# Optimization experiments

Hardware: AMD Instinct MI355X
Metric: run time of the kernel (lower is better)

## Reference

```python
import jax, jax.numpy as jnp
import numpy as np
from jax.scipy.special import logsumexp

N, S, D, C = 64, 512, 768, 32


def setup_inputs() -> dict:
    key = jax.random.key(0)
    k1, k2, k3, k4, k5 = jax.random.split(key, 5)
    X = jax.random.normal(k1, (N, S, D), dtype=jnp.float32)
    W = jax.random.normal(k2, (D, C), dtype=jnp.float32) * 0.02
    T = jax.random.normal(k3, (C, C), dtype=jnp.float32) * 0.1
    # one-hot labels [N,S,C]
    lab_idx = jax.random.randint(k4, (N, S), 0, C)
    labels = jax.nn.one_hot(lab_idx, C, dtype=jnp.float32)
    # pad_mask: 1 for first `length` positions, 0 after (lengths in [S//2, S])
    lengths = jax.random.randint(k5, (N,), S // 2, S + 1)
    pad_mask = (jnp.arange(S)[None, :] < lengths[:, None]).astype(jnp.float32)
    return {"X": X, "W": W, "T": T, "labels": labels, "pad_mask": pad_mask}


def _crf_nll(X, W, T, labels, pad_mask):
    npots = jnp.einsum("nsd,dc->nsc", X, W)  # [N,S,C]
    m = pad_mask[..., None]                   # [N,S,1]

    # Faithful replication of the in-place masking loop:
    # prev starts as the ORIGINAL last timestep (t-1 == -1 at t=0 in torch).
    def prop(prev, xs):
        nt, mt = xs
        new = (1.0 - mt) * prev + mt * nt
        return new, new

    _, np_t = jax.lax.scan(
        prop, npots[:, -1, :],
        (jnp.swapaxes(npots, 0, 1), jnp.swapaxes(m, 0, 1)))
    npots = jnp.swapaxes(np_t, 0, 1)  # [N,S,C]

    # Backward messages: msgs[i,j] = lse_k(np[i+1,k] + T[j,k] + msgs[i+1,k]) * mask[i+1]
    def bwd(msg_next, xs):
        np_next, m_next = xs  # [N,C], [N,1]
        new = logsumexp(np_next[:, None, :] + T[None, :, :] + msg_next[:, None, :],
                        axis=-1) * m_next
        return new, new

    xs = (jnp.swapaxes(npots[:, 1:, :], 0, 1), jnp.swapaxes(m[:, 1:, :], 0, 1))
    init = jnp.zeros((npots.shape[0], npots.shape[2]), dtype=npots.dtype)
    _, msgs = jax.lax.scan(bwd, init, xs, reverse=True)
    bwd0 = msgs[0]  # message at position 0

    logZ = logsumexp(npots[:, 0, :] + bwd0, axis=-1)  # [N]

    # Unnormalized gold-path score
    score = jnp.sum(jnp.sum(npots * labels, axis=-1) * pad_mask, axis=-1)
    labels_idx = jnp.argmax(labels, axis=-1)          # [N,S]
    trans = T[labels_idx[:, :-1]]                     # [N,S-1,C]
    score = score + jnp.sum(
        jnp.sum(trans * labels[:, 1:, :], axis=-1) * pad_mask[:, 1:], axis=-1)

    return -jnp.mean(score - logZ)


def reference(X, W, T, labels, pad_mask):
    return _crf_nll(X, W, T, labels, pad_mask)
```

## Files before the change

### kernel.cpp

```cpp
#include <hip/hip_runtime.h>
#include <hip/hip_bf16.h>
#include <math.h>

#define N_ 64
#define S_ 512
#define D_ 768
#define C_ 32
#define KCH 16
#define LC 32
#define WT_LD 776
#define BKC 96
#define ROWS_PB 128

typedef __attribute__((ext_vector_type(8))) short bf16x8;
typedef __attribute__((ext_vector_type(4))) float f32x4;
typedef __attribute__((ext_vector_type(16))) float f32x16;

__device__ inline ushort f2bf(float x) {
    unsigned int b = __builtin_bit_cast(unsigned int, x);
    return (ushort)((b + 0x7FFFu + ((b >> 16) & 1u)) >> 16);
}

__device__ inline unsigned cvt_pk_bf16(float lo, float hi) {
    unsigned r;
    asm("v_cvt_pk_bf16_f32 %0, %1, %2" : "=v"(r) : "v"(lo), "v"(hi));
    return r;
}

__device__ __forceinline__ void gload_lds16(const float* g, float* l) {
    __builtin_amdgcn_global_load_lds(
        (const __attribute__((address_space(1))) unsigned int*)g,
        (__attribute__((address_space(3))) unsigned int*)l, 16, 0, 0);
}

__global__ __launch_bounds__(512) void gemm_npots_mfma(const float* __restrict__ X,
                                                       const float* __restrict__ W,
                                                       float* __restrict__ npots) {
    __shared__ float  Xs[2][ROWS_PB * BKC];
    __shared__ ushort WtS[C_ * WT_LD];
    const int tid = threadIdx.x;
    const int w   = tid >> 6;
    const int l   = tid & 63;
    const int lr  = l & 15;
    const int q   = l >> 4;
    const int row0 = blockIdx.x * ROWS_PB;

    for (int i = tid; i < D_ * C_; i += 512) {
        const int k = i >> 5, c = i & 31;
        WtS[c * WT_LD + k] = f2bf(W[i]);
    }

    #define STAGE(ck, buf)                                                        \
        {                                                                         \
            _Pragma("unroll")                                                     \
            for (int i_ = 0; i_ < 6; ++i_) {                                      \
                const int G   = (w * 6 + i_) * 64 + l;                            \
                const int row = G / 24;                                           \
                const int g   = G - row * 24;                                     \
                const int gs  = g ^ (row & 7);                                    \
                gload_lds16(X + (size_t)(row0 + row) * D_ + (ck) * BKC + gs * 4,  \
                            &Xs[buf][G * 4]);                                     \
            }                                                                     \
        }

    STAGE(0, 0);
    asm volatile("s_waitcnt vmcnt(0)" ::: "memory");
    __syncthreads();

    f32x4 acc0 = {0.f, 0.f, 0.f, 0.f};
    f32x4 acc1 = {0.f, 0.f, 0.f, 0.f};
    const int myrow = w * 16 + lr;
    const int sw    = myrow & 7;
    const ushort* wb0 = &WtS[lr * WT_LD];
    const ushort* wb1 = &WtS[(lr + 16) * WT_LD];

    for (int c = 0; c < D_ / BKC; ++c) {
        if (c < D_ / BKC - 1) STAGE(c + 1, (c + 1) & 1);
        const float* xb = Xs[c & 1];
        #pragma unroll
        for (int kk = 0; kk < 3; ++kk) {
            const int g0 = 8 * kk + 2 * q;
            const f32x4 alo = *(const f32x4*)&xb[(myrow * 24 + (g0 ^ sw)) * 4];
            const f32x4 ahi = *(const f32x4*)&xb[(myrow * 24 + ((g0 + 1) ^ sw)) * 4];
            union { unsigned u[4]; bf16x8 v; } af;
            af.u[0] = cvt_pk_bf16(alo[0], alo[1]);
            af.u[1] = cvt_pk_bf16(alo[2], alo[3]);
            af.u[2] = cvt_pk_bf16(ahi[0], ahi[1]);
            af.u[3] = cvt_pk_bf16(ahi[2], ahi[3]);
            const int kg = c * BKC + kk * 32 + q * 8;
            const bf16x8 b0 = *(const bf16x8*)(wb0 + kg);
            const bf16x8 b1 = *(const bf16x8*)(wb1 + kg);
            acc0 = __builtin_amdgcn_mfma_f32_16x16x32_bf16(af.v, b0, acc0, 0, 0, 0);
            acc1 = __builtin_amdgcn_mfma_f32_16x16x32_bf16(af.v, b1, acc1, 0, 0, 0);
        }
        asm volatile("s_waitcnt vmcnt(0)" ::: "memory");
        __syncthreads();
    }
    #undef STAGE

    const int r0 = row0 + w * 16 + q * 4;
    #pragma unroll
    for (int reg = 0; reg < 4; ++reg) {
        npots[(size_t)(r0 + reg) * C_ + lr]      = acc0[reg];
        npots[(size_t)(r0 + reg) * C_ + lr + 16] = acc1[reg];
    }
}

__global__ __launch_bounds__(128) void chunk_score(const float* __restrict__ npots,
                                                   const float* __restrict__ pad,
                                                   const float* __restrict__ T,
                                                   const float* __restrict__ labels,
                                                   float* __restrict__ Bg,
                                                   float* __restrict__ chunk_ls,
                                                   float* __restrict__ scores_p) {
    const int n = blockIdx.x, k = blockIdx.y;
    const int tid = threadIdx.x;
    const int l = tid & 63;
    __shared__ __align__(16) float e_lds[LC * C_];

    if (tid >= 64) {
        const int tb = k * LC;
        int best = 0;
        if (l <= LC) {
            const int t = tb - 1 + l;
            if (t >= 0) {
                const float* lrow = labels + ((size_t)n * S_ + t) * C_;
                float bv = lrow[0];
                #pragma unroll
                for (int c = 1; c < C_; ++c) {
                    const float x = lrow[c];
                    if (x > bv) { bv = x; best = c; }
                }
            }
        }
        const int cur = __shfl(best, l + 1);
        float v = 0.f;
        if (l < LC) {
            const int t = tb + l;
            const float p = pad[(size_t)n * S_ + t];
            v = p * npots[((size_t)n * S_ + t) * C_ + cur];
            if (t >= 1) v = fmaf(p, T[best * C_ + cur], v);
        }
        #pragma unroll
        for (int o = 32; o >= 1; o >>= 1) v += __shfl_xor(v, o);
        if (l == 0) scores_p[n * KCH + k] = v;
        return;
    }

    const int cc = l & 31;
    const int h  = l >> 5;

    const float* pm = pad + (size_t)n * S_;
    float ls = 0.f;
    for (int t = l; t < S_; t += 64) ls += pm[t];
    #pragma unroll
    for (int o = 32; o >= 1; o >>= 1) ls += __shfl_xor(ls, o);
    const int len = (int)(ls + 0.5f);

    float* Bout = Bg + ((size_t)n * KCH + k) * (C_ * C_);
    const int lo = k * LC;
    const int hi = min(lo + LC, len - 1);

    if (lo >= len - 1) {
        #pragma unroll
        for (int qq = 0; qq < 16; ++qq) {
            const int row = (qq & 3) + 8 * (qq >> 2) + 4 * h;
            Bout[row * C_ + cc] = (row == cc) ? 1.f : 0.f;
        }
        if (l == 0) chunk_ls[n * KCH + k] = 0.f;
        return;
    }

    const int cnt = hi - lo;

    const float* npn = npots + ((size_t)n * S_ + lo) * C_;
    for (int qd = l * 4; qd < cnt * C_; qd += 256) {
        const float4 v = *(const float4*)(npn + qd);
        *(float4*)&e_lds[qd] = make_float4(expf(v.x), expf(v.y), expf(v.z), expf(v.w));
    }
    asm volatile("s_waitcnt lgkmcnt(0)" ::: "memory");

    float glo[8], ghi[8];
    {
        const float* el = e_lds + (size_t)(cnt - 1) * C_;
        #pragma unroll
        for (int j = 0; j < 8; ++j) {
            const int kk = 8 * h + j;
            glo[j] = el[kk]      * expf(T[kk * C_ + cc]);
            ghi[j] = el[kk + 16] * expf(T[(kk + 16) * C_ + cc]);
        }
    }

    if (cnt == 1) {
        #pragma unroll
        for (int j = 0; j < 8; ++j) {
            Bout[(8 * h + j) * C_ + cc]      = glo[j];
            Bout[(8 * h + j + 16) * C_ + cc] = ghi[j];
        }
        if (l == 0) chunk_ls[n * KCH + k] = 0.f;
        return;
    }

    union { unsigned u[4]; bf16x8 v; } ETalo, ETahi, blo, bhi;
    #pragma unroll
    for (int t = 0; t < 4; ++t) {
        const int kk = 8 * h + 2 * t;
        ETalo.u[t] = cvt_pk_bf16(expf(T[cc * C_ + kk]),      expf(T[cc * C_ + kk + 1]));
        ETahi.u[t] = cvt_pk_bf16(expf(T[cc * C_ + kk + 16]), expf(T[cc * C_ + kk + 17]));
        blo.u[t]   = cvt_pk_bf16(glo[2 * t], glo[2 * t + 1]);
        bhi.u[t]   = cvt_pk_bf16(ghi[2 * t], ghi[2 * t + 1]);
    }

    float logscale = 0.f;
    int it = 0;
    for (int i = hi - 2; i >= lo; --i) {
        f32x16 d = {};
        d = __builtin_amdgcn_mfma_f32_32x32x16_bf16(ETalo.v, blo.v, d, 0, 0, 0);
        d = __builtin_amdgcn_mfma_f32_32x32x16_bf16(ETahi.v, bhi.v, d, 0, 0, 0);

        const float* ep = e_lds + (i - lo) * C_ + 4 * h;
        const float4 e0 = *(const float4*)(ep);
        const float4 e1 = *(const float4*)(ep + 8);
        const float4 e2 = *(const float4*)(ep + 16);
        const float4 e3 = *(const float4*)(ep + 24);
        float sd[16];
        sd[0]  = d[0]  * e0.x;  sd[1]  = d[1]  * e0.y;  sd[2]  = d[2]  * e0.z;  sd[3]  = d[3]  * e0.w;
        sd[4]  = d[4]  * e1.x;  sd[5]  = d[5]  * e1.y;  sd[6]  = d[6]  * e1.z;  sd[7]  = d[7]  * e1.w;
        sd[8]  = d[8]  * e2.x;  sd[9]  = d[9]  * e2.y;  sd[10] = d[10] * e2.z;  sd[11] = d[11] * e2.w;
        sd[12] = d[12] * e3.x;  sd[13] = d[13] * e3.y;  sd[14] = d[14] * e3.z;  sd[15] = d[15] * e3.w;

        if ((++it & 7) == 0) {
            float m = sd[0];
            #pragma unroll
            for (int qq = 1; qq < 16; ++qq) m = fmaxf(m, sd[qq]);
            #pragma unroll
            for (int o = 32; o >= 1; o >>= 1) m = fmaxf(m, __shfl_xor(m, o));
            logscale += logf(m);
            const float inv = 1.f / m;
            #pragma unroll
            for (int qq = 0; qq < 16; ++qq) sd[qq] *= inv;
        }

        if (i > lo) {
            const unsigned w0 = cvt_pk_bf16(sd[0],  sd[1]);
            const unsigned w1 = cvt_pk_bf16(sd[2],  sd[3]);
            const unsigned w2 = cvt_pk_bf16(sd[4],  sd[5]);
            const unsigned w3 = cvt_pk_bf16(sd[6],  sd[7]);
            const unsigned w4 = cvt_pk_bf16(sd[8],  sd[9]);
            const unsigned w5 = cvt_pk_bf16(sd[10], sd[11]);
            const unsigned w6 = cvt_pk_bf16(sd[12], sd[13]);
            const unsigned w7 = cvt_pk_bf16(sd[14], sd[15]);
            const unsigned x0 = (unsigned)__shfl_xor((int)w0, 32);
            const unsigned x1 = (unsigned)__shfl_xor((int)w1, 32);
            const unsigned x2 = (unsigned)__shfl_xor((int)w2, 32);
            const unsigned x3 = (unsigned)__shfl_xor((int)w3, 32);
            const unsigned x4 = (unsigned)__shfl_xor((int)w4, 32);
            const unsigned x5 = (unsigned)__shfl_xor((int)w5, 32);
            const unsigned x6 = (unsigned)__shfl_xor((int)w6, 32);
            const unsigned x7 = (unsigned)__shfl_xor((int)w7, 32);
            blo.u[0] = h ? x2 : w0;
            blo.u[1] = h ? x3 : w1;
            blo.u[2] = h ? w2 : x0;
            blo.u[3] = h ? w3 : x1;
            bhi.u[0] = h ? x6 : w4;
            bhi.u[1] = h ? x7 : w5;
            bhi.u[2] = h ? w6 : x4;
            bhi.u[3] = h ? w7 : x5;
        } else {
            #pragma unroll
            for (int qq = 0; qq < 16; ++qq)
                Bout[((qq & 3) + 8 * (qq >> 2) + 4 * h) * C_ + cc] = sd[qq];
        }
    }
    if (l == 0) chunk_ls[n * KCH + k] = logscale;
}

__global__ __launch_bounds__(64) void combine_logZ(const float* __restrict__ npots,
                                                   const float* __restrict__ pad,
                                                   const float* __restrict__ Bg,
                                                   const float* __restrict__ chunk_ls,
                                                   float* __restrict__ logZ) {
    const int n = blockIdx.x;
    const int l = threadIdx.x;
    const int r = l & 31;
    const int h = l >> 5;
    __shared__ __align__(16) float w_lds[32];

    const float* pm = pad + (size_t)n * S_;
    float ls = 0.f;
    for (int t = l; t < S_; t += 64) ls += pm[t];
    #pragma unroll
    for (int o = 32; o >= 1; o >>= 1) ls += __shfl_xor(ls, o);
    const int len = (int)(ls + 0.5f);

    float cls = (l < KCH) ? chunk_ls[n * KCH + l] : 0.f;
    #pragma unroll
    for (int o = 32; o >= 1; o >>= 1) cls += __shfl_xor(cls, o);

    const float np_last = npots[((size_t)n * S_ + (len - 1)) * C_ + r];
    float m0 = np_last;
    #pragma unroll
    for (int o = 32; o >= 1; o >>= 1) m0 = fmaxf(m0, __shfl_xor(m0, o));
    float logscale = m0 + cls;
    if (h == 0) w_lds[r] = expf(np_last - m0);
    __syncthreads();

    float bv[16];
    {
        const float* Brow = Bg + ((size_t)n * KCH + (KCH - 1)) * (C_ * C_) + r * C_ + h * 16;
        #pragma unroll
        for (int t = 0; t < 4; ++t) *(float4*)&bv[t * 4] = *(const float4*)(Brow + t * 4);
    }

    float sn = 0.f;
    for (int k = KCH - 1; k >= 0; --k) {
        float cb[16];
        #pragma unroll
        for (int t = 0; t < 16; ++t) cb[t] = bv[t];
        if (k > 0) {
            const float* Brow = Bg + ((size_t)n * KCH + (k - 1)) * (C_ * C_) + r * C_ + h * 16;
            #pragma unroll
            for (int t = 0; t < 4; ++t) *(float4*)&bv[t * 4] = *(const float4*)(Brow + t * 4);
        }
        float wv[16];
        #pragma unroll
        for (int t = 0; t < 4; ++t) *(float4*)&wv[t * 4] = *(const float4*)&w_lds[h * 16 + t * 4];
        float s = 0.f;
        #pragma unroll
        for (int t = 0; t < 16; ++t) s = fmaf(cb[t], wv[t], s);
        s += __shfl_xor(s, 32);

        float m = s;
        #pragma unroll
        for (int o = 16; o >= 1; o >>= 1) m = fmaxf(m, __shfl_xor(m, o));
        logscale += logf(m);
        sn = s / m;
        __syncthreads();
        if (h == 0) w_lds[r] = sn;
        __syncthreads();
    }

    float v = (h == 0) ? sn : 0.f;
    #pragma unroll
    for (int o = 32; o >= 1; o >>= 1) v += __shfl_xor(v, o);
    if (l == 0) logZ[n] = logf(v) + logscale;
}

__global__ __launch_bounds__(64) void finalize(const float* __restrict__ scores_p,
                                               const float* __restrict__ logZ,
                                               float* __restrict__ out) {
    const int l = threadIdx.x;
    float sc = 0.f;
    #pragma unroll
    for (int tb = 0; tb < KCH; ++tb) sc += scores_p[l * KCH + tb];
    float v = sc - logZ[l];
    #pragma unroll
    for (int o = 32; o >= 1; o >>= 1) v += __shfl_xor(v, o);
    if (l == 0) out[0] = -v / (float)N_;
}

extern "C" void kernel_launch(void* const* d_in, const int* in_sizes, int n_in,
                              void* d_out, int out_size, void* d_ws, size_t ws_size,
                              hipStream_t stream) {
    const float* X      = (const float*)d_in[0];
    const float* W      = (const float*)d_in[1];
    const float* T      = (const float*)d_in[2];
    const float* labels = (const float*)d_in[3];
    const float* pad    = (const float*)d_in[4];
    float* out = (float*)d_out;

    float* npots    = (float*)d_ws;
    float* Bg       = npots + (size_t)N_ * S_ * C_;
    float* chunk_ls = Bg + (size_t)N_ * KCH * C_ * C_;
    float* logZ     = chunk_ls + N_ * KCH;
    float* scores_p = logZ + N_;

    gemm_npots_mfma<<<(N_ * S_) / ROWS_PB, 512, 0, stream>>>(X, W, npots);
    chunk_score<<<dim3(N_, KCH), 128, 0, stream>>>(npots, pad, T, labels, Bg, chunk_ls, scores_p);
    combine_logZ<<<N_, 64, 0, stream>>>(npots, pad, Bg, chunk_ls, logZ);
    finalize<<<1, 64, 0, stream>>>(scores_p, logZ, out);
}
```

Measured before the change: 49.86 us.

## Fuse GEMM, chunk scan, logZ combine and finalize into one kernel

Merges the four launches into a single kernel. Each GEMM block keeps its npots tile in LDS and immediately runs the chunked transfer-matrix products and the gold-path score for its four chunks. The last block finishing each sequence, detected with an atomic counter, combines the chunk matrices into logZ, and a global counter picks the last block overall to write the final mean. The GEMM main loop also drops its per-iteration block barrier: it prefetches two stages ahead and uses per-wave waitcnts, which is safe because each wave loads only the rows it consumes. In exchange the kernel adds a memset and atomics/threadfences for the counters, and the serial combine step now runs inside the last block of each sequence.

```diff
diff --git a/kernel.cpp b/kernel.cpp
--- a/kernel.cpp
+++ b/kernel.cpp
@@ -11,6 +11,7 @@
 #define WT_LD 776
 #define BKC 96
 #define ROWS_PB 128
+#define NBLK ((N_ * S_) / ROWS_PB)
 
 typedef __attribute__((ext_vector_type(8))) short bf16x8;
 typedef __attribute__((ext_vector_type(4))) float f32x4;
@@ -33,22 +34,40 @@
         (__attribute__((address_space(3))) unsigned int*)l, 16, 0, 0);
 }
 
-__global__ __launch_bounds__(512) void gemm_npots_mfma(const float* __restrict__ X,
-                                                       const float* __restrict__ W,
-                                                       float* __restrict__ npots) {
+__global__ __launch_bounds__(512) void crf_fused(const float* __restrict__ X,
+                                                 const float* __restrict__ W,
+                                                 const float* __restrict__ T,
+                                                 const float* __restrict__ labels,
+                                                 const float* __restrict__ pad,
+                                                 float* __restrict__ npots,
+                                                 float* __restrict__ Bg,
+                                                 float* __restrict__ chunk_ls,
+                                                 float* __restrict__ scores_p,
+                                                 float* __restrict__ logZ,
+                                                 unsigned* __restrict__ cnt_n,
+                                                 unsigned* __restrict__ cnt_all,
+                                                 float* __restrict__ out) {
     __shared__ float  Xs[2][ROWS_PB * BKC];
     __shared__ ushort WtS[C_ * WT_LD];
+    __shared__ float  wcomb[32];
+    __shared__ int    flagA;
+
+    const int bid = blockIdx.x;
+    const int n   = bid >> 2;
+    const int sq  = bid & 3;
+    const int row0 = bid * ROWS_PB;
     const int tid = threadIdx.x;
     const int w   = tid >> 6;
     const int l   = tid & 63;
-    const int lr  = l & 15;
-    const int q   = l >> 4;
-    const int row0 = blockIdx.x * ROWS_PB;
 
     for (int i = tid; i < D_ * C_; i += 512) {
         const int k = i >> 5, c = i & 31;
         WtS[c * WT_LD + k] = f2bf(W[i]);
     }
+    __syncthreads();
+
+    const int lr = l & 15;
+    const int q  = l >> 4;
 
     #define STAGE(ck, buf)                                                        \
         {                                                                         \
@@ -64,8 +83,7 @@
         }
 
     STAGE(0, 0);
-    asm volatile("s_waitcnt vmcnt(0)" ::: "memory");
-    __syncthreads();
+    STAGE(1, 1);
 
     f32x4 acc0 = {0.f, 0.f, 0.f, 0.f};
     f32x4 acc1 = {0.f, 0.f, 0.f, 0.f};
@@ -75,7 +93,8 @@
     const ushort* wb1 = &WtS[(lr + 16) * WT_LD];
 
     for (int c = 0; c < D_ / BKC; ++c) {
-        if (c < D_ / BKC - 1) STAGE(c + 1, (c + 1) & 1);
+        if (c < D_ / BKC - 1) asm volatile("s_waitcnt vmcnt(6)" ::: "memory");
+        else                  asm volatile("s_waitcnt vmcnt(0)" ::: "memory");
         const float* xb = Xs[c & 1];
         #pragma unroll
         for (int kk = 0; kk < 3; ++kk) {
@@ -93,33 +112,157 @@
             acc0 = __builtin_amdgcn_mfma_f32_16x16x32_bf16(af.v, b0, acc0, 0, 0, 0);
             acc1 = __builtin_amdgcn_mfma_f32_16x16x32_bf16(af.v, b1, acc1, 0, 0, 0);
         }
-        asm volatile("s_waitcnt vmcnt(0)" ::: "memory");
-        __syncthreads();
+        if (c < D_ / BKC - 2) {
+            asm volatile("s_waitcnt lgkmcnt(0)" ::: "memory");
+            STAGE(c + 2, c & 1);
+        }
     }
     #undef STAGE
 
-    const int r0 = row0 + w * 16 + q * 4;
-    #pragma unroll
-    for (int reg = 0; reg < 4; ++reg) {
-        npots[(size_t)(r0 + reg) * C_ + lr]      = acc0[reg];
-        npots[(size_t)(r0 + reg) * C_ + lr + 16] = acc1[reg];
-    }
-}
-
-__global__ __launch_bounds__(128) void chunk_score(const float* __restrict__ npots,
-                                                   const float* __restrict__ pad,
-                                                   const float* __restrict__ T,
-                                                   const float* __restrict__ labels,
-                                                   float* __restrict__ Bg,
-                                                   float* __restrict__ chunk_ls,
-                                                   float* __restrict__ scores_p) {
-    const int n = blockIdx.x, k = blockIdx.y;
-    const int tid = threadIdx.x;
-    const int l = tid & 63;
-    __shared__ __align__(16) float e_lds[LC * C_];
-
-    if (tid >= 64) {
-        const int tb = k * LC;
+    __syncthreads();
+
+    float* np_s = (float*)&Xs[0][0];
+    float* e_s  = np_s + 128 * 33;
+    {
+        const int r0l = w * 16 + q * 4;
+        #pragma unroll
+        for (int reg = 0; reg < 4; ++reg) {
+            np_s[(r0l + reg) * 33 + lr]      = acc0[reg];
+            np_s[(r0l + reg) * 33 + lr + 16] = acc1[reg];
+            npots[(size_t)(row0 + r0l + reg) * C_ + lr]      = acc0[reg];
+            npots[(size_t)(row0 + r0l + reg) * C_ + lr + 16] = acc1[reg];
+        }
+    }
+    __syncthreads();
+
+    int len = 0;
+    if (w < 4) {
+        float lsum = 0.f;
+        for (int t = l; t < S_; t += 64) lsum += pad[(size_t)n * S_ + t];
+        #pragma unroll
+        for (int o = 32; o >= 1; o >>= 1) lsum += __shfl_xor(lsum, o);
+        len = (int)(lsum + 0.5f);
+
+        const int kg = sq * 4 + w;
+        const int lo = kg * LC;
+        float* Bout = Bg + ((size_t)n * KCH + kg) * (C_ * C_);
+        const int cc = l & 31;
+        const int h  = l >> 5;
+        const int hi = min(lo + LC, len - 1);
+
+        if (lo >= len - 1) {
+            #pragma unroll
+            for (int qq = 0; qq < 16; ++qq) {
+                const int row = (qq & 3) + 8 * (qq >> 2) + 4 * h;
+                Bout[row * C_ + cc] = (row == cc) ? 1.f : 0.f;
+            }
+            if (l == 0) chunk_ls[n * KCH + kg] = 0.f;
+        } else {
+            const int cnt = hi - lo;
+            float* ew = e_s + w * 1024;
+            for (int i = l; i < 1024; i += 64) {
+                const int rr = i >> 5, c2 = i & 31;
+                ew[i] = expf(np_s[(w * 32 + rr) * 33 + c2]);
+            }
+            asm volatile("s_waitcnt lgkmcnt(0)" ::: "memory");
+
+            float glo[8], ghi[8];
+            {
+                const float* el = ew + (size_t)(cnt - 1) * C_;
+                #pragma unroll
+                for (int j = 0; j < 8; ++j) {
+                    const int kk = 8 * h + j;
+                    glo[j] = el[kk]      * expf(T[kk * C_ + cc]);
+                    ghi[j] = el[kk + 16] * expf(T[(kk + 16) * C_ + cc]);
+                }
+            }
+
+            if (cnt == 1) {
+                #pragma unroll
+                for (int j = 0; j < 8; ++j) {
+                    Bout[(8 * h + j) * C_ + cc]      = glo[j];
+                    Bout[(8 * h + j + 16) * C_ + cc] = ghi[j];
+                }
+                if (l == 0) chunk_ls[n * KCH + kg] = 0.f;
+            } else {
+                union { unsigned u[4]; bf16x8 v; } ETalo, ETahi, blo, bhi;
+                #pragma unroll
+                for (int t = 0; t < 4; ++t) {
+                    const int kk = 8 * h + 2 * t;
+                    ETalo.u[t] = cvt_pk_bf16(expf(T[cc * C_ + kk]),      expf(T[cc * C_ + kk + 1]));
+                    ETahi.u[t] = cvt_pk_bf16(expf(T[cc * C_ + kk + 16]), expf(T[cc * C_ + kk + 17]));
+                    blo.u[t]   = cvt_pk_bf16(glo[2 * t], glo[2 * t + 1]);
+                    bhi.u[t]   = cvt_pk_bf16(ghi[2 * t], ghi[2 * t + 1]);
+                }
+
+                float logscale = 0.f;
+                int it = 0;
+                for (int i = hi - 2; i >= lo; --i) {
+                    f32x16 d = {};
+                    d = __builtin_amdgcn_mfma_f32_32x32x16_bf16(ETalo.v, blo.v, d, 0, 0, 0);
+                    d = __builtin_amdgcn_mfma_f32_32x32x16_bf16(ETahi.v, bhi.v, d, 0, 0, 0);
+
+                    const float* ep = ew + (i - lo) * C_ + 4 * h;
+                    const float4 e0 = *(const float4*)(ep);
+                    const float4 e1 = *(const float4*)(ep + 8);
+                    const float4 e2 = *(const float4*)(ep + 16);
+                    const float4 e3 = *(const float4*)(ep + 24);
+                    float sd[16];
+                    sd[0]  = d[0]  * e0.x;  sd[1]  = d[1]  * e0.y;  sd[2]  = d[2]  * e0.z;  sd[3]  = d[3]  * e0.w;
+                    sd[4]  = d[4]  * e1.x;  sd[5]  = d[5]  * e1.y;  sd[6]  = d[6]  * e1.z;  sd[7]  = d[7]  * e1.w;
+                    sd[8]  = d[8]  * e2.x;  sd[9]  = d[9]  * e2.y;  sd[10] = d[10] * e2.z;  sd[11] = d[11] * e2.w;
+                    sd[12] = d[12] * e3.x;  sd[13] = d[13] * e3.y;  sd[14] = d[14] * e3.z;  sd[15] = d[15] * e3.w;
+
+                    if ((++it & 7) == 0) {
+                        float m = sd[0];
+                        #pragma unroll
+                        for (int qq = 1; qq < 16; ++qq) m = fmaxf(m, sd[qq]);
+                        #pragma unroll
+                        for (int o = 32; o >= 1; o >>= 1) m = fmaxf(m, __shfl_xor(m, o));
+                        logscale += logf(m);
+                        const float inv = 1.f / m;
+                        #pragma unroll
+                        for (int qq = 0; qq < 16; ++qq) sd[qq] *= inv;
+                    }
+
+                    if (i > lo) {
+                        const unsigned w0 = cvt_pk_bf16(sd[0],  sd[1]);
+                        const unsigned w1 = cvt_pk_bf16(sd[2],  sd[3]);
+                        const unsigned w2 = cvt_pk_bf16(sd[4],  sd[5]);
+                        const unsigned w3 = cvt_pk_bf16(sd[6],  sd[7]);
+                        const unsigned w4 = cvt_pk_bf16(sd[8],  sd[9]);
+                        const unsigned w5 = cvt_pk_bf16(sd[10], sd[11]);
+                        const unsigned w6 = cvt_pk_bf16(sd[12], sd[13]);
+                        const unsigned w7 = cvt_pk_bf16(sd[14], sd[15]);
+                        const unsigned x0 = (unsigned)__shfl_xor((int)w0, 32);
+                        const unsigned x1 = (unsigned)__shfl_xor((int)w1, 32);
+                        const unsigned x2 = (unsigned)__shfl_xor((int)w2, 32);
+                        const unsigned x3 = (unsigned)__shfl_xor((int)w3, 32);
+                        const unsigned x4 = (unsigned)__shfl_xor((int)w4, 32);
+                        const unsigned x5 = (unsigned)__shfl_xor((int)w5, 32);
+                        const unsigned x6 = (unsigned)__shfl_xor((int)w6, 32);
+                        const unsigned x7 = (unsigned)__shfl_xor((int)w7, 32);
+                        blo.u[0] = h ? x2 : w0;
+                        blo.u[1] = h ? x3 : w1;
+                        blo.u[2] = h ? w2 : x0;
+                        blo.u[3] = h ? w3 : x1;
+                        bhi.u[0] = h ? x6 : w4;
+                        bhi.u[1] = h ? x7 : w5;
+                        bhi.u[2] = h ? w6 : x4;
+                        bhi.u[3] = h ? w7 : x5;
+                    } else {
+                        #pragma unroll
+                        for (int qq = 0; qq < 16; ++qq)
+                            Bout[((qq & 3) + 8 * (qq >> 2) + 4 * h) * C_ + cc] = sd[qq];
+                    }
+                }
+                if (l == 0) chunk_ls[n * KCH + kg] = logscale;
+            }
+        }
+    } else {
+        const int wv = w - 4;
+        const int kg = sq * 4 + wv;
+        const int tb = kg * LC;
         int best = 0;
         if (l <= LC) {
             const int t = tb - 1 + l;
@@ -138,225 +281,88 @@
         if (l < LC) {
             const int t = tb + l;
             const float p = pad[(size_t)n * S_ + t];
-            v = p * npots[((size_t)n * S_ + t) * C_ + cur];
+            v = p * np_s[(wv * 32 + l) * 33 + cur];
             if (t >= 1) v = fmaf(p, T[best * C_ + cur], v);
         }
         #pragma unroll
         for (int o = 32; o >= 1; o >>= 1) v += __shfl_xor(v, o);
-        if (l == 0) scores_p[n * KCH + k] = v;
-        return;
-    }
-
-    const int cc = l & 31;
-    const int h  = l >> 5;
-
-    const float* pm = pad + (size_t)n * S_;
-    float ls = 0.f;
-    for (int t = l; t < S_; t += 64) ls += pm[t];
-    #pragma unroll
-    for (int o = 32; o >= 1; o >>= 1) ls += __shfl_xor(ls, o);
-    const int len = (int)(ls + 0.5f);
-
-    float* Bout = Bg + ((size_t)n * KCH + k) * (C_ * C_);
-    const int lo = k * LC;
-    const int hi = min(lo + LC, len - 1);
-
-    if (lo >= len - 1) {
-        #pragma unroll
-        for (int qq = 0; qq < 16; ++qq) {
-            const int row = (qq & 3) + 8 * (qq >> 2) + 4 * h;
-            Bout[row * C_ + cc] = (row == cc) ? 1.f : 0.f;
-        }
-        if (l == 0) chunk_ls[n * KCH + k] = 0.f;
-        return;
-    }
-
-    const int cnt = hi - lo;
-
-    const float* npn = npots + ((size_t)n * S_ + lo) * C_;
-    for (int qd = l * 4; qd < cnt * C_; qd += 256) {
-        const float4 v = *(const float4*)(npn + qd);
-        *(float4*)&e_lds[qd] = make_float4(expf(v.x), expf(v.y), expf(v.z), expf(v.w));
-    }
-    asm volatile("s_waitcnt lgkmcnt(0)" ::: "memory");
-
-    float glo[8], ghi[8];
-    {
-        const float* el = e_lds + (size_t)(cnt - 1) * C_;
-        #pragma unroll
-        for (int j = 0; j < 8; ++j) {
-            const int kk = 8 * h + j;
-            glo[j] = el[kk]      * expf(T[kk * C_ + cc]);
-            ghi[j] = el[kk + 16] * expf(T[(kk + 16) * C_ + cc]);
-        }
-    }
-
-    if (cnt == 1) {
-        #pragma unroll
-        for (int j = 0; j < 8; ++j) {
-            Bout[(8 * h + j) * C_ + cc]      = glo[j];
-            Bout[(8 * h + j + 16) * C_ + cc] = ghi[j];
-        }
-        if (l == 0) chunk_ls[n * KCH + k] = 0.f;
-        return;
-    }
-
-    union { unsigned u[4]; bf16x8 v; } ETalo, ETahi, blo, bhi;
-    #pragma unroll
-    for (int t = 0; t < 4; ++t) {
-        const int kk = 8 * h + 2 * t;
-        ETalo.u[t] = cvt_pk_bf16(expf(T[cc * C_ + kk]),      expf(T[cc * C_ + kk + 1]));
-        ETahi.u[t] = cvt_pk_bf16(expf(T[cc * C_ + kk + 16]), expf(T[cc * C_ + kk + 17]));
-        blo.u[t]   = cvt_pk_bf16(glo[2 * t], glo[2 * t + 1]);
-        bhi.u[t]   = cvt_pk_bf16(ghi[2 * t], ghi[2 * t + 1]);
-    }
-
-    float logscale = 0.f;
-    int it = 0;
-    for (int i = hi - 2; i >= lo; --i) {
-        f32x16 d = {};
-        d = __builtin_amdgcn_mfma_f32_32x32x16_bf16(ETalo.v, blo.v, d, 0, 0, 0);
-        d = __builtin_amdgcn_mfma_f32_32x32x16_bf16(ETahi.v, bhi.v, d, 0, 0, 0);
-
-        const float* ep = e_lds + (i - lo) * C_ + 4 * h;
-        const float4 e0 = *(const float4*)(ep);
-        const float4 e1 = *(const float4*)(ep + 8);
-        const float4 e2 = *(const float4*)(ep + 16);
-        const float4 e3 = *(const float4*)(ep + 24);
-        float sd[16];
-        sd[0]  = d[0]  * e0.x;  sd[1]  = d[1]  * e0.y;  sd[2]  = d[2]  * e0.z;  sd[3]  = d[3]  * e0.w;
-        sd[4]  = d[4]  * e1.x;  sd[5]  = d[5]  * e1.y;  sd[6]  = d[6]  * e1.z;  sd[7]  = d[7]  * e1.w;
-        sd[8]  = d[8]  * e2.x;  sd[9]  = d[9]  * e2.y;  sd[10] = d[10] * e2.z;  sd[11] = d[11] * e2.w;
-        sd[12] = d[12] * e3.x;  sd[13] = d[13] * e3.y;  sd[14] = d[14] * e3.z;  sd[15] = d[15] * e3.w;
-
-        if ((++it & 7) == 0) {
-            float m = sd[0];
-            #pragma unroll
-            for (int qq = 1; qq < 16; ++qq) m = fmaxf(m, sd[qq]);
-            #pragma unroll
-            for (int o = 32; o >= 1; o >>= 1) m = fmaxf(m, __shfl_xor(m, o));
-            logscale += logf(m);
-            const float inv = 1.f / m;
-            #pragma unroll
-            for (int qq = 0; qq < 16; ++qq) sd[qq] *= inv;
-        }
-
-        if (i > lo) {
-            const unsigned w0 = cvt_pk_bf16(sd[0],  sd[1]);
-            const unsigned w1 = cvt_pk_bf16(sd[2],  sd[3]);
-            const unsigned w2 = cvt_pk_bf16(sd[4],  sd[5]);
-            const unsigned w3 = cvt_pk_bf16(sd[6],  sd[7]);
-            const unsigned w4 = cvt_pk_bf16(sd[8],  sd[9]);
-            const unsigned w5 = cvt_pk_bf16(sd[10], sd[11]);
-            const unsigned w6 = cvt_pk_bf16(sd[12], sd[13]);
-            const unsigned w7 = cvt_pk_bf16(sd[14], sd[15]);
-            const unsigned x0 = (unsigned)__shfl_xor((int)w0, 32);
-            const unsigned x1 = (unsigned)__shfl_xor((int)w1, 32);
-            const unsigned x2 = (unsigned)__shfl_xor((int)w2, 32);
-            const unsigned x3 = (unsigned)__shfl_xor((int)w3, 32);
-            const unsigned x4 = (unsigned)__shfl_xor((int)w4, 32);
-            const unsigned x5 = (unsigned)__shfl_xor((int)w5, 32);
-            const unsigned x6 = (unsigned)__shfl_xor((int)w6, 32);
-            const unsigned x7 = (unsigned)__shfl_xor((int)w7, 32);
-            blo.u[0] = h ? x2 : w0;
-            blo.u[1] = h ? x3 : w1;
-            blo.u[2] = h ? w2 : x0;
-            blo.u[3] = h ? w3 : x1;
-            bhi.u[0] = h ? x6 : w4;
-            bhi.u[1] = h ? x7 : w5;
-            bhi.u[2] = h ? w6 : x4;
-            bhi.u[3] = h ? w7 : x5;
-        } else {
-            #pragma unroll
-            for (int qq = 0; qq < 16; ++qq)
-                Bout[((qq & 3) + 8 * (qq >> 2) + 4 * h) * C_ + cc] = sd[qq];
-        }
-    }
-    if (l == 0) chunk_ls[n * KCH + k] = logscale;
-}
-
-__global__ __launch_bounds__(64) void combine_logZ(const float* __restrict__ npots,
-                                                   const float* __restrict__ pad,
-                                                   const float* __restrict__ Bg,
-                                                   const float* __restrict__ chunk_ls,
-                                                   float* __restrict__ logZ) {
-    const int n = blockIdx.x;
-    const int l = threadIdx.x;
-    const int r = l & 31;
-    const int h = l >> 5;
-    __shared__ __align__(16) float w_lds[32];
-
-    const float* pm = pad + (size_t)n * S_;
-    float ls = 0.f;
-    for (int t = l; t < S_; t += 64) ls += pm[t];
-    #pragma unroll
-    for (int o = 32; o >= 1; o >>= 1) ls += __shfl_xor(ls, o);
-    const int len = (int)(ls + 0.5f);
-
-    float cls = (l < KCH) ? chunk_ls[n * KCH + l] : 0.f;
-    #pragma unroll
-    for (int o = 32; o >= 1; o >>= 1) cls += __shfl_xor(cls, o);
-
-    const float np_last = npots[((size_t)n * S_ + (len - 1)) * C_ + r];
-    float m0 = np_last;
-    #pragma unroll
-    for (int o = 32; o >= 1; o >>= 1) m0 = fmaxf(m0, __shfl_xor(m0, o));
-    float logscale = m0 + cls;
-    if (h == 0) w_lds[r] = expf(np_last - m0);
-    __syncthreads();
-
-    float bv[16];
-    {
-        const float* Brow = Bg + ((size_t)n * KCH + (KCH - 1)) * (C_ * C_) + r * C_ + h * 16;
-        #pragma unroll
-        for (int t = 0; t < 4; ++t) *(float4*)&bv[t * 4] = *(const float4*)(Brow + t * 4);
-    }
-
-    float sn = 0.f;
-    for (int k = KCH - 1; k >= 0; --k) {
-        float cb[16];
-        #pragma unroll
-        for (int t = 0; t < 16; ++t) cb[t] = bv[t];
-        if (k > 0) {
-            const float* Brow = Bg + ((size_t)n * KCH + (k - 1)) * (C_ * C_) + r * C_ + h * 16;
-            #pragma unroll
-            for (int t = 0; t < 4; ++t) *(float4*)&bv[t * 4] = *(const float4*)(Brow + t * 4);
-        }
-        float wv[16];
-        #pragma unroll
-        for (int t = 0; t < 4; ++t) *(float4*)&wv[t * 4] = *(const float4*)&w_lds[h * 16 + t * 4];
-        float s = 0.f;
-        #pragma unroll
-        for (int t = 0; t < 16; ++t) s = fmaf(cb[t], wv[t], s);
-        s += __shfl_xor(s, 32);
-
-        float m = s;
-        #pragma unroll
-        for (int o = 16; o >= 1; o >>= 1) m = fmaxf(m, __shfl_xor(m, o));
-        logscale += logf(m);
-        sn = s / m;
+        if (l == 0) scores_p[n * KCH + kg] = v;
+    }
+
+    __syncthreads();
+    __threadfence();
+    if (tid == 0) flagA = (atomicAdd(&cnt_n[n], 1u) == 3u) ? 1 : 0;
+    __syncthreads();
+
+    if (flagA) {
+        __threadfence();
+        if (w == 0) {
+            const int r  = l & 31;
+            const int hh = l >> 5;
+            float cls = (l < KCH) ? chunk_ls[n * KCH + l] : 0.f;
+            #pragma unroll
+            for (int o = 32; o >= 1; o >>= 1) cls += __shfl_xor(cls, o);
+
+            const float np_last = npots[((size_t)n * S_ + (len - 1)) * C_ + r];
+            float m0 = np_last;
+            #pragma unroll
+            for (int o = 32; o >= 1; o >>= 1) m0 = fmaxf(m0, __shfl_xor(m0, o));
+            float logscale = m0 + cls;
+            if (hh == 0) wcomb[r] = expf(np_last - m0);
+            asm volatile("s_waitcnt lgkmcnt(0)" ::: "memory");
+
+            float bv[16];
+            {
+                const float* Brow = Bg + ((size_t)n * KCH + (KCH - 1)) * (C_ * C_) + r * C_ + hh * 16;
+                #pragma unroll
+                for (int t = 0; t < 4; ++t) *(float4*)&bv[t * 4] = *(const float4*)(Brow + t * 4);
+            }
+            float sn = 0.f;
+            for (int k2 = KCH - 1; k2 >= 0; --k2) {
+                float cb[16];
+                #pragma unroll
+                for (int t = 0; t < 16; ++t) cb[t] = bv[t];
+                if (k2 > 0) {
+                    const float* Br2 = Bg + ((size_t)n * KCH + (k2 - 1)) * (C_ * C_) + r * C_ + hh * 16;
+                    #pragma unroll
+                    for (int t = 0; t < 4; ++t) *(float4*)&bv[t * 4] = *(const float4*)(Br2 + t * 4);
+                }
+                float wv2[16];
+                #pragma unroll
+                for (int t = 0; t < 4; ++t) *(float4*)&wv2[t * 4] = *(const float4*)&wcomb[hh * 16 + t * 4];
+                float s = 0.f;
+                #pragma unroll
+                for (int t = 0; t < 16; ++t) s = fmaf(cb[t], wv2[t], s);
+                s += __shfl_xor(s, 32);
+
+                float m = s;
+                #pragma unroll
+                for (int o = 16; o >= 1; o >>= 1) m = fmaxf(m, __shfl_xor(m, o));
+                logscale += logf(m);
+                sn = s / m;
+                if (hh == 0) wcomb[r] = sn;
+                asm volatile("s_waitcnt lgkmcnt(0)" ::: "memory");
+            }
+            float vz = (hh == 0) ? sn : 0.f;
+            #pragma unroll
+            for (int o = 32; o >= 1; o >>= 1) vz += __shfl_xor(vz, o);
+            if (l == 0) logZ[n] = logf(vz) + logscale;
+        }
+        __threadfence();
         __syncthreads();
-        if (h == 0) w_lds[r] = sn;
+        if (tid == 0) flagA = (atomicAdd(cnt_all, 1u) == 63u) ? 1 : 0;
         __syncthreads();
-    }
-
-    float v = (h == 0) ? sn : 0.f;
-    #pragma unroll
-    for (int o = 32; o >= 1; o >>= 1) v += __shfl_xor(v, o);
-    if (l == 0) logZ[n] = logf(v) + logscale;
-}
-
-__global__ __launch_bounds__(64) void finalize(const float* __restrict__ scores_p,
-                                               const float* __restrict__ logZ,
-                                               float* __restrict__ out) {
-    const int l = threadIdx.x;
-    float sc = 0.f;
-    #pragma unroll
-    for (int tb = 0; tb < KCH; ++tb) sc += scores_p[l * KCH + tb];
-    float v = sc - logZ[l];
-    #pragma unroll
-    for (int o = 32; o >= 1; o >>= 1) v += __shfl_xor(v, o);
-    if (l == 0) out[0] = -v / (float)N_;
+        if (flagA && w == 0) {
+            __threadfence();
+            float sc = 0.f;
+            #pragma unroll
+            for (int tb2 = 0; tb2 < KCH; ++tb2) sc += scores_p[l * KCH + tb2];
+            float v2 = sc - logZ[l];
+            #pragma unroll
+            for (int o = 32; o >= 1; o >>= 1) v2 += __shfl_xor(v2, o);
+            if (l == 0) out[0] = -v2 / (float)N_;
+        }
+    }
 }
 
 extern "C" void kernel_launch(void* const* d_in, const int* in_sizes, int n_in,
@@ -369,14 +375,16 @@
     const float* pad    = (const float*)d_in[4];
     float* out = (float*)d_out;
 
-    float* npots    = (float*)d_ws;
-    float* Bg       = npots + (size_t)N_ * S_ * C_;
-    float* chunk_ls = Bg + (size_t)N_ * KCH * C_ * C_;
-    float* logZ     = chunk_ls + N_ * KCH;
-    float* scores_p = logZ + N_;
-
-    gemm_npots_mfma<<<(N_ * S_) / ROWS_PB, 512, 0, stream>>>(X, W, npots);
-    chunk_score<<<dim3(N_, KCH), 128, 0, stream>>>(npots, pad, T, labels, Bg, chunk_ls, scores_p);
-    combine_logZ<<<N_, 64, 0, stream>>>(npots, pad, Bg, chunk_ls, logZ);
-    finalize<<<1, 64, 0, stream>>>(scores_p, logZ, out);
-}
+    float*    npots    = (float*)d_ws;
+    float*    Bg       = npots + (size_t)N_ * S_ * C_;
+    float*    chunk_ls = Bg + (size_t)N_ * KCH * C_ * C_;
+    float*    logZ     = chunk_ls + N_ * KCH;
+    float*    scores_p = logZ + N_;
+    unsigned* cnt_n    = (unsigned*)(scores_p + 1024);
+    unsigned* cnt_all  = cnt_n + N_;
+
+    hipMemsetAsync(cnt_n, 0, (N_ + 1) * sizeof(unsigned), stream);
+
+    crf_fused<<<NBLK, 512, 0, stream>>>(X, W, T, labels, pad, npots, Bg, chunk_ls,
+                                        scores_p, logZ, cnt_n, cnt_all, out);
+}
```

Measured after the change: 131.5 us. +163.8%, slower.
